# Kernel tuning notes

Hardware: AMD Instinct MI355X
Metric: run time of the kernel (lower is better)

## Reference

```python
import jax, jax.numpy as jnp
import numpy as np


def setup_inputs() -> dict:
    key = jax.random.key(0)
    k1, k2, k3 = jax.random.split(key, 3)
    D, L = 1024, 8192
    Bsz = 4
    h = jax.random.normal(k1, (D, L), dtype=jnp.float32)
    x = jax.random.normal(k2, (Bsz, D, L), dtype=jnp.float32)
    B = jax.random.normal(k3, (D, 1), dtype=jnp.float32)
    return {"h": h, "x": x, "B": B}


def reference(h, x, B):
    L = h.shape[-1]
    n = 2 * L  # zero-pad to 2L for linear (non-circular) convolution
    # torch rfft(norm='forward') divides by n; irfft(norm='forward') multiplies
    # by n — the factors cancel, and jnp supports the same norm argument.
    h_f = jnp.fft.rfft(h.astype(jnp.float32), n=n, norm="forward")  # [D, L+1]
    x_f = jnp.fft.rfft(x.astype(h.dtype), n=n)                      # [Bsz, D, L+1]
    y = jnp.fft.irfft(h_f * x_f, n=n, norm="forward")[..., :L]
    y = y + x * B  # B broadcasts [D,1] over [Bsz, D, L]
    return y.astype(x.dtype)
```

## Files before the change

kernel.cpp:

```cpp
#include <hip/hip_runtime.h>
#include <math.h>


#define FFT_N  8192
#define LOG_N  13
#define SEQ_L  8192
#define DIM_D  1024
#define NTHR   512

__device__ __forceinline__ float2 cadd(float2 a, float2 b){ return make_float2(a.x+b.x, a.y+b.y); }
__device__ __forceinline__ float2 csub(float2 a, float2 b){ return make_float2(a.x-b.x, a.y-b.y); }
__device__ __forceinline__ float2 cmul(float2 a, float2 b){ return make_float2(a.x*b.x - a.y*b.y, a.x*b.y + a.y*b.x); }
__device__ __forceinline__ int rev13(int k){ return (int)(__brev((unsigned)k) >> 19); }
__device__ __forceinline__ int SW(int i){ return i ^ ((i >> 5) & 15) ^ ((i >> 9) & 15); }

__device__ __forceinline__ void dif_pass4(float2 v[16], float2 w){
    {   constexpr float c8c[8] = {1.f, 0.92387953251f, 0.70710678119f, 0.38268343236f, 0.f, -0.38268343236f, -0.70710678119f, -0.92387953251f};
        constexpr float c8s[8] = {0.f, -0.38268343236f, -0.70710678119f, -0.92387953251f, -1.f, -0.92387953251f, -0.70710678119f, -0.38268343236f};
        #pragma unroll
        for (int m = 0; m < 8; ++m){
            float2 tw = cmul(make_float2(c8c[m], c8s[m]), w);
            float2 u = v[m], t = v[m+8];
            v[m] = cadd(u,t);
            v[m+8] = cmul(csub(u,t), tw);
        }
    }
    w = cmul(w,w);
    {   constexpr float c4c[4] = {1.f, 0.70710678119f, 0.f, -0.70710678119f};
        constexpr float c4s[4] = {0.f, -0.70710678119f, -1.f, -0.70710678119f};
        #pragma unroll
        for (int h = 0; h < 16; h += 8)
            #pragma unroll
            for (int m = 0; m < 4; ++m){
                float2 tw = cmul(make_float2(c4c[m], c4s[m]), w);
                float2 u = v[h+m], t = v[h+m+4];
                v[h+m] = cadd(u,t);
                v[h+m+4] = cmul(csub(u,t), tw);
            }
    }
    w = cmul(w,w);
    #pragma unroll
    for (int q = 0; q < 16; q += 4)
        #pragma unroll
        for (int m = 0; m < 2; ++m){
            float2 tw = (m == 0) ? w : make_float2(w.y, -w.x);
            float2 u = v[q+m], t = v[q+m+2];
            v[q+m] = cadd(u,t);
            v[q+m+2] = cmul(csub(u,t), tw);
        }
    w = cmul(w,w);
    #pragma unroll
    for (int e = 0; e < 16; e += 2){
        float2 u = v[e], t = v[e+1];
        v[e] = cadd(u,t);
        v[e+1] = cmul(csub(u,t), w);
    }
}

__device__ __forceinline__ void dit_pass4(float2 v[16], float2 w3){
    float2 w2 = cmul(w3,w3), w1 = cmul(w2,w2), w0 = cmul(w1,w1);
    #pragma unroll
    for (int e = 0; e < 16; e += 2){
        float2 t = cmul(v[e+1], w0);
        float2 u = v[e];
        v[e] = cadd(u,t); v[e+1] = csub(u,t);
    }
    #pragma unroll
    for (int q = 0; q < 16; q += 4)
        #pragma unroll
        for (int m = 0; m < 2; ++m){
            float2 tw = (m == 0) ? w1 : make_float2(-w1.y, w1.x);
            float2 t = cmul(v[q+m+2], tw);
            float2 u = v[q+m];
            v[q+m] = cadd(u,t); v[q+m+2] = csub(u,t);
        }
    {   constexpr float c4c[4] = {1.f, 0.70710678119f, 0.f, -0.70710678119f};
        constexpr float c4s[4] = {0.f, 0.70710678119f, 1.f, 0.70710678119f};
        #pragma unroll
        for (int h = 0; h < 16; h += 8)
            #pragma unroll
            for (int m = 0; m < 4; ++m){
                float2 tw = cmul(make_float2(c4c[m], c4s[m]), w2);
                float2 t = cmul(v[h+m+4], tw);
                float2 u = v[h+m];
                v[h+m] = cadd(u,t); v[h+m+4] = csub(u,t);
            }
    }
    {   constexpr float c8c[8] = {1.f, 0.92387953251f, 0.70710678119f, 0.38268343236f, 0.f, -0.38268343236f, -0.70710678119f, -0.92387953251f};
        constexpr float c8s[8] = {0.f, 0.38268343236f, 0.70710678119f, 0.92387953251f, 1.f, 0.92387953251f, 0.70710678119f, 0.38268343236f};
        #pragma unroll
        for (int m = 0; m < 8; ++m){
            float2 tw = cmul(make_float2(c8c[m], c8s[m]), w3);
            float2 t = cmul(v[m+8], tw);
            float2 u = v[m];
            v[m] = cadd(u,t); v[m+8] = csub(u,t);
        }
    }
}

__device__ __forceinline__ void fwd_fft12(float2* z, int tid){
    float2 v[16];
    float sn, cs;
    __sincosf(-(float)M_PI * (float)tid * (1.0f/4096.0f), &sn, &cs);
    float2 base = make_float2(cs, sn);
    #pragma unroll
    for (int k = 0; k < 16; ++k) v[k] = z[SW((k<<9) | tid)];
    dif_pass4(v, base);
    #pragma unroll
    for (int k = 0; k < 16; ++k) z[SW((k<<9) | tid)] = v[k];
    __syncthreads();
    const int hi = tid >> 5, lo = tid & 31;
    __sincosf(-(float)M_PI * (float)lo * (1.0f/256.0f), &sn, &cs);
    base = make_float2(cs, sn);
    #pragma unroll
    for (int k = 0; k < 16; ++k) v[k] = z[SW((hi<<9) | (k<<5) | lo)];
    dif_pass4(v, base);
    #pragma unroll
    for (int k = 0; k < 16; ++k) z[SW((hi<<9) | (k<<5) | lo)] = v[k];
    __syncthreads();
    const int h2 = tid >> 1, b0 = tid & 1;
    base = b0 ? make_float2(0.98078528040f, -0.19509032202f)
              : make_float2(1.f, 0.f);
    #pragma unroll
    for (int k = 0; k < 16; ++k) v[k] = z[SW((h2<<5) | (k<<1) | b0)];
    dif_pass4(v, base);
    #pragma unroll
    for (int k = 0; k < 16; ++k) z[SW((h2<<5) | (k<<1) | b0)] = v[k];
    __syncthreads();
}

__device__ __forceinline__ void untangle(float2 zk, float2 znk, float2 t, float2& A, float2& G){
    float2 E  = make_float2(0.5f*(zk.x+znk.x), 0.5f*(zk.y-znk.y));
    float2 O  = make_float2(0.5f*(zk.y+znk.y), -0.5f*(zk.x-znk.x));
    float2 tO = cmul(t, O);
    A = cadd(E, tO); G = csub(E, tO);
}

__device__ __forceinline__ void pointmul(float2 zk, float2 znk, float2 t,
                                         float2 Ah, float2 Gh, float invN,
                                         float2& Wp, float2& Wm){
    float2 Xp, Xm; untangle(zk, znk, t, Xp, Xm);
    float2 Cp = cmul(Ah, Xp), Cm = cmul(Gh, Xm);
    float2 S  = make_float2(0.5f*(Cp.x+Cm.x), 0.5f*(Cp.y+Cm.y));
    float2 Dd = make_float2(0.5f*(Cp.x-Cm.x), 0.5f*(Cp.y-Cm.y));
    float2 u  = make_float2(t.y*Dd.x - t.x*Dd.y, t.y*Dd.y + t.x*Dd.x);
    Wp = make_float2((S.x+u.x)*invN, (S.y+u.y)*invN);
    Wm = make_float2((S.x-u.x)*invN, -((S.y-u.y)*invN));
}

__global__ __launch_bounds__(NTHR)
void h_spec_kernel(const float* __restrict__ h,
                   float4* __restrict__ p0, float4* __restrict__ p1,
                   float2* __restrict__ hs2)
{
    __shared__ float2 z[FFT_N];
    const int tid = (int)threadIdx.x;
    const int d   = (int)blockIdx.x;
    const float2* hrow = (const float2*)(h + (size_t)d * SEQ_L);

    #pragma unroll
    for (int j = 0; j < 8; ++j){
        int n = tid + NTHR * j;
        z[SW(n)] = hrow[n];
        z[SW(n + FFT_N/2)] = make_float2(0.f, 0.f);
    }
    __syncthreads();
    fwd_fft12(z, tid);

    const size_t base = (size_t)d * 2048;
    #pragma unroll
    for (int q = 0; q < 4; ++q){
        int g = tid + NTHR * q;
        float2 A1, G1, A2, G2;
        if (g == 0){
            float2 z0 = z[SW(0)], z1 = z[SW(1)], z2 = z[SW(2)], z3 = z[SW(3)];
            float2 Z0 = cadd(z0,z1), Z1 = csub(z0,z1), Z2 = cadd(z2,z3), Z3 = csub(z2,z3);
            float2 A3, G3;
            untangle(Z0, Z0, make_float2(1.f, 0.f), A1, G1);
            untangle(Z2, Z3, make_float2(0.70710678119f, -0.70710678119f), A2, G2);
            untangle(Z1, Z1, make_float2(0.f, -1.f), A3, G3);
            hs2[(size_t)d*2 + 0] = A3;
            hs2[(size_t)d*2 + 1] = G3;
        } else {
            int a = rev13(g), c = rev13(4096 - g);
            float2 za = z[SW(a)], zb = z[SW(a+1)], zc = z[SW(c)], zd = z[SW(c+1)];
            float2 Z12a = cadd(za,zb), Z12b = csub(za,zb);
            float2 Z12c = cadd(zc,zd), Z12d = csub(zc,zd);
            float sn, cs; __sincosf(-(float)M_PI * (float)g * (1.0f/8192.0f), &sn, &cs);
            float2 t1 = make_float2(cs, sn), t2 = make_float2(-sn, -cs);
            untangle(Z12a, Z12d, t1, A1, G1);
            untangle(Z12c, Z12b, t2, A2, G2);
        }
        p0[base + q*NTHR + tid] = make_float4(A1.x, A1.y, G1.x, G1.y);
        p1[base + q*NTHR + tid] = make_float4(A2.x, A2.y, G2.x, G2.y);
    }
}

__global__ __launch_bounds__(NTHR)
void fftconv_x_kernel(const float* __restrict__ x,
                      const float* __restrict__ Bv,
                      float* __restrict__ y,
                      const float4* __restrict__ p0, const float4* __restrict__ p1,
                      const float2* __restrict__ hs2)
{
    __shared__ float2 z[FFT_N];
    const int tid = (int)threadIdx.x;
    const int d   = (int)blockIdx.x;
    const int b   = (int)blockIdx.y;

    const float Bd = Bv[d];
    const float2* xrow = (const float2*)(x + ((size_t)b * DIM_D + (size_t)d) * SEQ_L);
    float2*       yrow = (float2*)(y + ((size_t)b * DIM_D + (size_t)d) * SEQ_L);
    const float invN = 1.0f / (float)FFT_N;

    #pragma unroll
    for (int j = 0; j < 8; ++j){
        int n = tid + NTHR * j;
        z[SW(n)] = xrow[n];
        z[SW(n + FFT_N/2)] = make_float2(0.f, 0.f);
    }
    __syncthreads();
    fwd_fft12(z, tid);

    const size_t base = (size_t)d * 2048;
    #pragma unroll
    for (int q = 0; q < 4; ++q){
        int g = tid + NTHR * q;
        float4 f0 = p0[base + q*NTHR + tid];
        float4 f1 = p1[base + q*NTHR + tid];
        float2 Ah1 = make_float2(f0.x, f0.y), Gh1 = make_float2(f0.z, f0.w);
        float2 Ah2 = make_float2(f1.x, f1.y), Gh2 = make_float2(f1.z, f1.w);
        if (g == 0){
            float2 A3 = hs2[(size_t)d*2 + 0], G3 = hs2[(size_t)d*2 + 1];
            float2 z0 = z[SW(0)], z1 = z[SW(1)], z2 = z[SW(2)], z3 = z[SW(3)];
            float2 Z0 = cadd(z0,z1), Z1 = csub(z0,z1), Z2 = cadd(z2,z3), Z3 = csub(z2,z3);
            float2 W0, W0b, W1, W1b, W2, W3;
            pointmul(Z0, Z0, make_float2(1.f, 0.f),  Ah1, Gh1, invN, W0, W0b);
            pointmul(Z1, Z1, make_float2(0.f, -1.f), A3,  G3,  invN, W1, W1b);
            pointmul(Z2, Z3, make_float2(0.70710678119f, -0.70710678119f), Ah2, Gh2, invN, W2, W3);
            z[SW(0)] = cadd(W0, W1);
            z[SW(1)] = csub(W0, W1);
            z[SW(2)] = cadd(W2, W3);
            z[SW(3)] = csub(W2, W3);
        } else {
            int a = rev13(g), c = rev13(4096 - g);
            float2 za = z[SW(a)], zb = z[SW(a+1)], zc = z[SW(c)], zd = z[SW(c+1)];
            float2 Z12a = cadd(za,zb), Z12b = csub(za,zb);
            float2 Z12c = cadd(zc,zd), Z12d = csub(zc,zd);
            float sn, cs; __sincosf(-(float)M_PI * (float)g * (1.0f/8192.0f), &sn, &cs);
            float2 t1 = make_float2(cs, sn), t2 = make_float2(-sn, -cs);
            float2 Wp1, Wm1, Wp2, Wm2;
            pointmul(Z12a, Z12d, t1, Ah1, Gh1, invN, Wp1, Wm1);
            pointmul(Z12c, Z12b, t2, Ah2, Gh2, invN, Wp2, Wm2);
            z[SW(a)]   = cadd(Wp1, Wm2);
            z[SW(a+1)] = csub(Wp1, Wm2);
            z[SW(c)]   = cadd(Wp2, Wm1);
            z[SW(c+1)] = csub(Wp2, Wm1);
        }
    }
    __syncthreads();

    {
        float2 v[16];
        float sn, cs;
        const int h2 = tid >> 1, b0 = tid & 1, hi = tid >> 5, lo = tid & 31;
        float2 w3 = b0 ? make_float2(0.98078528040f, 0.19509032202f)
                       : make_float2(1.f, 0.f);
        #pragma unroll
        for (int k = 0; k < 16; ++k) v[k] = z[SW((h2<<5) | (k<<1) | b0)];
        dit_pass4(v, w3);
        #pragma unroll
        for (int k = 0; k < 16; ++k) z[SW((h2<<5) | (k<<1) | b0)] = v[k];
        __syncthreads();
        __sincosf((float)M_PI * (float)lo * (1.0f/256.0f), &sn, &cs);
        w3 = make_float2(cs, sn);
        #pragma unroll
        for (int k = 0; k < 16; ++k) v[k] = z[SW((hi<<9) | (k<<5) | lo)];
        dit_pass4(v, w3);
        #pragma unroll
        for (int k = 0; k < 16; ++k) z[SW((hi<<9) | (k<<5) | lo)] = v[k];
        __syncthreads();
        __sincosf((float)M_PI * (float)tid * (1.0f/4096.0f), &sn, &cs);
        w3 = make_float2(cs, sn);
        #pragma unroll
        for (int k = 0; k < 16; ++k) v[k] = z[SW((k<<9) | tid)];
        dit_pass4(v, w3);
        #pragma unroll
        for (int k = 0; k < 16; ++k) z[SW((k<<9) | tid)] = v[k];
        __syncthreads();
    }

    #pragma unroll
    for (int j = 0; j < 8; ++j){
        int n = tid + NTHR * j;
        float2 wv = z[SW(n)];
        float2 xv = xrow[n];
        yrow[n] = make_float2(wv.x + xv.x * Bd, wv.y + xv.y * Bd);
    }
}

__global__ __launch_bounds__(NTHR)
void fftconv_fused(const float* __restrict__ h,
                   const float* __restrict__ x,
                   const float* __restrict__ Bv,
                   float* __restrict__ y)
{
    __shared__ float2 z[FFT_N];
    const int tid = (int)threadIdx.x;
    const int d   = (int)blockIdx.x;
    const int b   = (int)blockIdx.y;

    const float Bd = Bv[d];
    const float2* hrow = (const float2*)(h + (size_t)d * SEQ_L);
    const float2* xrow = (const float2*)(x + ((size_t)b * DIM_D + (size_t)d) * SEQ_L);
    float2*       yrow = (float2*)(y + ((size_t)b * DIM_D + (size_t)d) * SEQ_L);
    const float invN = 1.0f / (float)FFT_N;

    #pragma unroll
    for (int j = 0; j < 8; ++j){
        int n = tid + NTHR * j;
        z[SW(n)] = hrow[n];
        z[SW(n + FFT_N/2)] = make_float2(0.f, 0.f);
    }
    __syncthreads();
    fwd_fft12(z, tid);

    float2 Ah1[4], Gh1[4], Ah2[4], Gh2[4], Ah3, Gh3;
    #pragma unroll
    for (int q = 0; q < 4; ++q){
        int g = tid + NTHR * q;
        if (g == 0){
            float2 z0 = z[SW(0)], z1 = z[SW(1)], z2 = z[SW(2)], z3 = z[SW(3)];
            float2 Z0 = cadd(z0,z1), Z1 = csub(z0,z1), Z2 = cadd(z2,z3), Z3 = csub(z2,z3);
            untangle(Z0, Z0, make_float2(1.f, 0.f), Ah1[0], Gh1[0]);
            untangle(Z2, Z3, make_float2(0.70710678119f, -0.70710678119f), Ah2[0], Gh2[0]);
            untangle(Z1, Z1, make_float2(0.f, -1.f), Ah3, Gh3);
        } else {
            int a = rev13(g), c = rev13(4096 - g);
            float2 za = z[SW(a)], zb = z[SW(a+1)], zc = z[SW(c)], zd = z[SW(c+1)];
            float2 Z12a = cadd(za,zb), Z12b = csub(za,zb);
            float2 Z12c = cadd(zc,zd), Z12d = csub(zc,zd);
            float sn, cs; __sincosf(-(float)M_PI * (float)g * (1.0f/8192.0f), &sn, &cs);
            float2 t1 = make_float2(cs, sn), t2 = make_float2(-sn, -cs);
            untangle(Z12a, Z12d, t1, Ah1[q], Gh1[q]);
            untangle(Z12c, Z12b, t2, Ah2[q], Gh2[q]);
        }
    }
    __syncthreads();

    #pragma unroll
    for (int j = 0; j < 8; ++j){
        int n = tid + NTHR * j;
        z[SW(n)] = xrow[n];
        z[SW(n + FFT_N/2)] = make_float2(0.f, 0.f);
    }
    __syncthreads();
    fwd_fft12(z, tid);

    #pragma unroll
    for (int q = 0; q < 4; ++q){
        int g = tid + NTHR * q;
        if (g == 0){
            float2 z0 = z[SW(0)], z1 = z[SW(1)], z2 = z[SW(2)], z3 = z[SW(3)];
            float2 Z0 = cadd(z0,z1), Z1 = csub(z0,z1), Z2 = cadd(z2,z3), Z3 = csub(z2,z3);
            float2 W0, W0b, W1, W1b, W2, W3;
            pointmul(Z0, Z0, make_float2(1.f, 0.f),  Ah1[0], Gh1[0], invN, W0, W0b);
            pointmul(Z1, Z1, make_float2(0.f, -1.f), Ah3,    Gh3,    invN, W1, W1b);
            pointmul(Z2, Z3, make_float2(0.70710678119f, -0.70710678119f), Ah2[0], Gh2[0], invN, W2, W3);
            z[SW(0)] = cadd(W0, W1);
            z[SW(1)] = csub(W0, W1);
            z[SW(2)] = cadd(W2, W3);
            z[SW(3)] = csub(W2, W3);
        } else {
            int a = rev13(g), c = rev13(4096 - g);
            float2 za = z[SW(a)], zb = z[SW(a+1)], zc = z[SW(c)], zd = z[SW(c+1)];
            float2 Z12a = cadd(za,zb), Z12b = csub(za,zb);
            float2 Z12c = cadd(zc,zd), Z12d = csub(zc,zd);
            float sn, cs; __sincosf(-(float)M_PI * (float)g * (1.0f/8192.0f), &sn, &cs);
            float2 t1 = make_float2(cs, sn), t2 = make_float2(-sn, -cs);
            float2 Wp1, Wm1, Wp2, Wm2;
            pointmul(Z12a, Z12d, t1, Ah1[q], Gh1[q], invN, Wp1, Wm1);
            pointmul(Z12c, Z12b, t2, Ah2[q], Gh2[q], invN, Wp2, Wm2);
            z[SW(a)]   = cadd(Wp1, Wm2);
            z[SW(a+1)] = csub(Wp1, Wm2);
            z[SW(c)]   = cadd(Wp2, Wm1);
            z[SW(c+1)] = csub(Wp2, Wm1);
        }
    }
    __syncthreads();

    {
        float2 v[16];
        float sn, cs;
        const int h2 = tid >> 1, b0 = tid & 1, hi = tid >> 5, lo = tid & 31;
        float2 w3 = b0 ? make_float2(0.98078528040f, 0.19509032202f)
                       : make_float2(1.f, 0.f);
        #pragma unroll
        for (int k = 0; k < 16; ++k) v[k] = z[SW((h2<<5) | (k<<1) | b0)];
        dit_pass4(v, w3);
        #pragma unroll
        for (int k = 0; k < 16; ++k) z[SW((h2<<5) | (k<<1) | b0)] = v[k];
        __syncthreads();
        __sincosf((float)M_PI * (float)lo * (1.0f/256.0f), &sn, &cs);
        w3 = make_float2(cs, sn);
        #pragma unroll
        for (int k = 0; k < 16; ++k) v[k] = z[SW((hi<<9) | (k<<5) | lo)];
        dit_pass4(v, w3);
        #pragma unroll
        for (int k = 0; k < 16; ++k) z[SW((hi<<9) | (k<<5) | lo)] = v[k];
        __syncthreads();
        __sincosf((float)M_PI * (float)tid * (1.0f/4096.0f), &sn, &cs);
        w3 = make_float2(cs, sn);
        #pragma unroll
        for (int k = 0; k < 16; ++k) v[k] = z[SW((k<<9) | tid)];
        dit_pass4(v, w3);
        #pragma unroll
        for (int k = 0; k < 16; ++k) z[SW((k<<9) | tid)] = v[k];
        __syncthreads();
    }

    #pragma unroll
    for (int j = 0; j < 8; ++j){
        int n = tid + NTHR * j;
        float2 wv = z[SW(n)];
        float2 xv = xrow[n];
        yrow[n] = make_float2(wv.x + xv.x * Bd, wv.y + xv.y * Bd);
    }
}

extern "C" void kernel_launch(void* const* d_in, const int* in_sizes, int n_in,
                              void* d_out, int out_size, void* d_ws, size_t ws_size,
                              hipStream_t stream) {
    const float* h  = (const float*)d_in[0];
    const float* x  = (const float*)d_in[1];
    const float* Bv = (const float*)d_in[2];
    float* y = (float*)d_out;

    const int bsz = out_size / (DIM_D * SEQ_L);
    const size_t plane = (size_t)DIM_D * 2048;
    const size_t need  = plane * 2 * sizeof(float4) + (size_t)DIM_D * 2 * sizeof(float2);

    if (ws_size >= need) {
        float4* p0  = (float4*)d_ws;
        float4* p1  = p0 + plane;
        float2* hs2 = (float2*)(p1 + plane);
        hipLaunchKernelGGL(h_spec_kernel, dim3(DIM_D), dim3(NTHR), 0, stream, h, p0, p1, hs2);
        hipLaunchKernelGGL(fftconv_x_kernel, dim3(DIM_D, bsz), dim3(NTHR), 0, stream,
                           x, Bv, y, p0, p1, hs2);
    } else {
        hipLaunchKernelGGL(fftconv_fused, dim3(DIM_D, bsz), dim3(NTHR), 0, stream, h, x, Bv, y);
    }
}
```

Before: 408.3 us.

## Fuse global load into first FFT pass and epilogue into last pass

The first radix-16 DIF pass now reads the input row directly from global memory into registers. Because the upper half of the input is zero padding, that first stage reduces to a twiddle multiply, so no zero-filled shared-memory load or extra barrier is needed. The final inverse pass writes y = conv + x*B straight from registers, and in the batched kernel it reuses the input values kept in registers instead of re-reading x. Swizzle index math is specialised per pass and trivial twiddles are special-cased. This removes one shared-memory round trip and two barriers per FFT, at the cost of higher register pressure from the saved x values.

Result: faster. 378.1 us (-7.4%).

```diff
diff --git a/kernel.cpp b/kernel.cpp
--- a/kernel.cpp
+++ b/kernel.cpp
@@ -3,7 +3,6 @@
 
 
 #define FFT_N  8192
-#define LOG_N  13
 #define SEQ_L  8192
 #define DIM_D  1024
 #define NTHR   512
@@ -14,47 +13,63 @@
 __device__ __forceinline__ int rev13(int k){ return (int)(__brev((unsigned)k) >> 19); }
 __device__ __forceinline__ int SW(int i){ return i ^ ((i >> 5) & 15) ^ ((i >> 9) & 15); }
 
+__device__ __forceinline__ float2 tw8_dif(int m, float2 w){
+    constexpr float c[8] = {1.f, 0.92387953251f, 0.70710678119f, 0.38268343236f, 0.f, -0.38268343236f, -0.70710678119f, -0.92387953251f};
+    constexpr float s[8] = {0.f, -0.38268343236f, -0.70710678119f, -0.92387953251f, -1.f, -0.92387953251f, -0.70710678119f, -0.38268343236f};
+    if (m == 0) return w;
+    if (m == 4) return make_float2(w.y, -w.x);
+    return cmul(make_float2(c[m], s[m]), w);
+}
+__device__ __forceinline__ float2 tw8_dit(int m, float2 w){
+    constexpr float c[8] = {1.f, 0.92387953251f, 0.70710678119f, 0.38268343236f, 0.f, -0.38268343236f, -0.70710678119f, -0.92387953251f};
+    constexpr float s[8] = {0.f, 0.38268343236f, 0.70710678119f, 0.92387953251f, 1.f, 0.92387953251f, 0.70710678119f, 0.38268343236f};
+    if (m == 0) return w;
+    if (m == 4) return make_float2(-w.y, w.x);
+    return cmul(make_float2(c[m], s[m]), w);
+}
+
+__device__ __forceinline__ void dif_stage8(float2 v[16], float2 w){
+    #pragma unroll
+    for (int m = 0; m < 8; ++m){
+        float2 tw = tw8_dif(m, w);
+        float2 u = v[m], t = v[m+8];
+        v[m] = cadd(u,t);
+        v[m+8] = cmul(csub(u,t), tw);
+    }
+}
+
+__device__ __forceinline__ void dif_tail3(float2 v[16], float2 w){
+    {
+        float2 t0 = w;
+        float2 t1 = cmul(make_float2(0.70710678119f, -0.70710678119f), w);
+        float2 t2 = make_float2(w.y, -w.x);
+        float2 t3 = cmul(make_float2(-0.70710678119f, -0.70710678119f), w);
+        #pragma unroll
+        for (int h = 0; h < 16; h += 8){
+            { float2 u=v[h+0], t=v[h+4]; v[h+0]=cadd(u,t); v[h+4]=cmul(csub(u,t), t0); }
+            { float2 u=v[h+1], t=v[h+5]; v[h+1]=cadd(u,t); v[h+5]=cmul(csub(u,t), t1); }
+            { float2 u=v[h+2], t=v[h+6]; v[h+2]=cadd(u,t); v[h+6]=cmul(csub(u,t), t2); }
+            { float2 u=v[h+3], t=v[h+7]; v[h+3]=cadd(u,t); v[h+7]=cmul(csub(u,t), t3); }
+        }
+    }
+    w = cmul(w,w);
+    #pragma unroll
+    for (int q = 0; q < 16; q += 4){
+        { float2 u=v[q+0], t=v[q+2]; v[q+0]=cadd(u,t); v[q+2]=cmul(csub(u,t), w); }
+        { float2 u=v[q+1], t=v[q+3]; float2 tw=make_float2(w.y,-w.x);
+          v[q+1]=cadd(u,t); v[q+3]=cmul(csub(u,t), tw); }
+    }
+    w = cmul(w,w);
+    #pragma unroll
+    for (int e = 0; e < 16; e += 2){
+        float2 u=v[e], t=v[e+1];
+        v[e]=cadd(u,t); v[e+1]=cmul(csub(u,t), w);
+    }
+}
+
 __device__ __forceinline__ void dif_pass4(float2 v[16], float2 w){
-    {   constexpr float c8c[8] = {1.f, 0.92387953251f, 0.70710678119f, 0.38268343236f, 0.f, -0.38268343236f, -0.70710678119f, -0.92387953251f};
-        constexpr float c8s[8] = {0.f, -0.38268343236f, -0.70710678119f, -0.92387953251f, -1.f, -0.92387953251f, -0.70710678119f, -0.38268343236f};
-        #pragma unroll
-        for (int m = 0; m < 8; ++m){
-            float2 tw = cmul(make_float2(c8c[m], c8s[m]), w);
-            float2 u = v[m], t = v[m+8];
-            v[m] = cadd(u,t);
-            v[m+8] = cmul(csub(u,t), tw);
-        }
-    }
-    w = cmul(w,w);
-    {   constexpr float c4c[4] = {1.f, 0.70710678119f, 0.f, -0.70710678119f};
-        constexpr float c4s[4] = {0.f, -0.70710678119f, -1.f, -0.70710678119f};
-        #pragma unroll
-        for (int h = 0; h < 16; h += 8)
-            #pragma unroll
-            for (int m = 0; m < 4; ++m){
-                float2 tw = cmul(make_float2(c4c[m], c4s[m]), w);
-                float2 u = v[h+m], t = v[h+m+4];
-                v[h+m] = cadd(u,t);
-                v[h+m+4] = cmul(csub(u,t), tw);
-            }
-    }
-    w = cmul(w,w);
-    #pragma unroll
-    for (int q = 0; q < 16; q += 4)
-        #pragma unroll
-        for (int m = 0; m < 2; ++m){
-            float2 tw = (m == 0) ? w : make_float2(w.y, -w.x);
-            float2 u = v[q+m], t = v[q+m+2];
-            v[q+m] = cadd(u,t);
-            v[q+m+2] = cmul(csub(u,t), tw);
-        }
-    w = cmul(w,w);
-    #pragma unroll
-    for (int e = 0; e < 16; e += 2){
-        float2 u = v[e], t = v[e+1];
-        v[e] = cadd(u,t);
-        v[e+1] = cmul(csub(u,t), w);
-    }
+    dif_stage8(v, w);
+    dif_tail3(v, cmul(w,w));
 }
 
 __device__ __forceinline__ void dit_pass4(float2 v[16], float2 w3){
@@ -66,66 +81,72 @@
         v[e] = cadd(u,t); v[e+1] = csub(u,t);
     }
     #pragma unroll
-    for (int q = 0; q < 16; q += 4)
-        #pragma unroll
-        for (int m = 0; m < 2; ++m){
-            float2 tw = (m == 0) ? w1 : make_float2(-w1.y, w1.x);
-            float2 t = cmul(v[q+m+2], tw);
-            float2 u = v[q+m];
-            v[q+m] = cadd(u,t); v[q+m+2] = csub(u,t);
-        }
-    {   constexpr float c4c[4] = {1.f, 0.70710678119f, 0.f, -0.70710678119f};
-        constexpr float c4s[4] = {0.f, 0.70710678119f, 1.f, 0.70710678119f};
-        #pragma unroll
-        for (int h = 0; h < 16; h += 8)
-            #pragma unroll
-            for (int m = 0; m < 4; ++m){
-                float2 tw = cmul(make_float2(c4c[m], c4s[m]), w2);
-                float2 t = cmul(v[h+m+4], tw);
-                float2 u = v[h+m];
-                v[h+m] = cadd(u,t); v[h+m+4] = csub(u,t);
-            }
-    }
-    {   constexpr float c8c[8] = {1.f, 0.92387953251f, 0.70710678119f, 0.38268343236f, 0.f, -0.38268343236f, -0.70710678119f, -0.92387953251f};
-        constexpr float c8s[8] = {0.f, 0.38268343236f, 0.70710678119f, 0.92387953251f, 1.f, 0.92387953251f, 0.70710678119f, 0.38268343236f};
-        #pragma unroll
-        for (int m = 0; m < 8; ++m){
-            float2 tw = cmul(make_float2(c8c[m], c8s[m]), w3);
-            float2 t = cmul(v[m+8], tw);
-            float2 u = v[m];
-            v[m] = cadd(u,t); v[m+8] = csub(u,t);
-        }
-    }
-}
-
-__device__ __forceinline__ void fwd_fft12(float2* z, int tid){
+    for (int q = 0; q < 16; q += 4){
+        { float2 t = cmul(v[q+2], w1); float2 u=v[q+0]; v[q+0]=cadd(u,t); v[q+2]=csub(u,t); }
+        { float2 tw = make_float2(-w1.y, w1.x);
+          float2 t = cmul(v[q+3], tw); float2 u=v[q+1]; v[q+1]=cadd(u,t); v[q+3]=csub(u,t); }
+    }
+    {   float2 t0 = w2;
+        float2 t1 = cmul(make_float2(0.70710678119f, 0.70710678119f), w2);
+        float2 t2 = make_float2(-w2.y, w2.x);
+        float2 t3 = cmul(make_float2(-0.70710678119f, 0.70710678119f), w2);
+        #pragma unroll
+        for (int h = 0; h < 16; h += 8){
+            { float2 t=cmul(v[h+4], t0); float2 u=v[h+0]; v[h+0]=cadd(u,t); v[h+4]=csub(u,t); }
+            { float2 t=cmul(v[h+5], t1); float2 u=v[h+1]; v[h+1]=cadd(u,t); v[h+5]=csub(u,t); }
+            { float2 t=cmul(v[h+6], t2); float2 u=v[h+2]; v[h+2]=cadd(u,t); v[h+6]=csub(u,t); }
+            { float2 t=cmul(v[h+7], t3); float2 u=v[h+3]; v[h+3]=cadd(u,t); v[h+7]=csub(u,t); }
+        }
+    }
+    #pragma unroll
+    for (int m = 0; m < 8; ++m){
+        float2 tw = tw8_dit(m, w3);
+        float2 t = cmul(v[m+8], tw);
+        float2 u = v[m];
+        v[m] = cadd(u,t); v[m+8] = csub(u,t);
+    }
+}
+
+template<bool SAVEX>
+__device__ __forceinline__ void fwd_fft12_fused(float2* z, const float2* __restrict__ row,
+                                                int tid, float2* xs){
     float2 v[16];
     float sn, cs;
     __sincosf(-(float)M_PI * (float)tid * (1.0f/4096.0f), &sn, &cs);
-    float2 base = make_float2(cs, sn);
-    #pragma unroll
-    for (int k = 0; k < 16; ++k) v[k] = z[SW((k<<9) | tid)];
-    dif_pass4(v, base);
-    #pragma unroll
-    for (int k = 0; k < 16; ++k) z[SW((k<<9) | tid)] = v[k];
-    __syncthreads();
+    float2 w = make_float2(cs, sn);
+    const int T1 = tid ^ ((tid >> 5) & 15);
+    #pragma unroll
+    for (int k = 0; k < 8; ++k){
+        v[k] = row[(k<<9) | tid];
+        if (SAVEX) xs[k] = v[k];
+    }
+    #pragma unroll
+    for (int m = 0; m < 8; ++m) v[m+8] = cmul(v[m], tw8_dif(m, w));
+    dif_tail3(v, cmul(w,w));
+    #pragma unroll
+    for (int k = 0; k < 16; ++k) z[(k<<9) | (T1 ^ k)] = v[k];
+    __syncthreads();
+
     const int hi = tid >> 5, lo = tid & 31;
+    const int baseB = hi << 9, TB = lo ^ hi;
     __sincosf(-(float)M_PI * (float)lo * (1.0f/256.0f), &sn, &cs);
-    base = make_float2(cs, sn);
-    #pragma unroll
-    for (int k = 0; k < 16; ++k) v[k] = z[SW((hi<<9) | (k<<5) | lo)];
-    dif_pass4(v, base);
-    #pragma unroll
-    for (int k = 0; k < 16; ++k) z[SW((hi<<9) | (k<<5) | lo)] = v[k];
-    __syncthreads();
+    w = make_float2(cs, sn);
+    #pragma unroll
+    for (int k = 0; k < 16; ++k) v[k] = z[baseB | (k<<5) | (TB ^ k)];
+    dif_pass4(v, w);
+    #pragma unroll
+    for (int k = 0; k < 16; ++k) z[baseB | (k<<5) | (TB ^ k)] = v[k];
+    __syncthreads();
+
     const int h2 = tid >> 1, b0 = tid & 1;
-    base = b0 ? make_float2(0.98078528040f, -0.19509032202f)
-              : make_float2(1.f, 0.f);
-    #pragma unroll
-    for (int k = 0; k < 16; ++k) v[k] = z[SW((h2<<5) | (k<<1) | b0)];
-    dif_pass4(v, base);
-    #pragma unroll
-    for (int k = 0; k < 16; ++k) z[SW((h2<<5) | (k<<1) | b0)] = v[k];
+    const int baseC = h2 << 5, M3 = (h2 ^ (h2 >> 4)) & 15;
+    w = b0 ? make_float2(0.98078528040f, -0.19509032202f)
+           : make_float2(1.f, 0.f);
+    #pragma unroll
+    for (int k = 0; k < 16; ++k) v[k] = z[baseC | (((k<<1)|b0) ^ M3)];
+    dif_pass4(v, w);
+    #pragma unroll
+    for (int k = 0; k < 16; ++k) z[baseC | (((k<<1)|b0) ^ M3)] = v[k];
     __syncthreads();
 }
 
@@ -158,14 +179,8 @@
     const int d   = (int)blockIdx.x;
     const float2* hrow = (const float2*)(h + (size_t)d * SEQ_L);
 
-    #pragma unroll
-    for (int j = 0; j < 8; ++j){
-        int n = tid + NTHR * j;
-        z[SW(n)] = hrow[n];
-        z[SW(n + FFT_N/2)] = make_float2(0.f, 0.f);
-    }
-    __syncthreads();
-    fwd_fft12(z, tid);
+    float2 dummy[8];
+    fwd_fft12_fused<false>(z, hrow, tid, dummy);
 
     const size_t base = (size_t)d * 2048;
     #pragma unroll
@@ -213,14 +228,8 @@
     float2*       yrow = (float2*)(y + ((size_t)b * DIM_D + (size_t)d) * SEQ_L);
     const float invN = 1.0f / (float)FFT_N;
 
-    #pragma unroll
-    for (int j = 0; j < 8; ++j){
-        int n = tid + NTHR * j;
-        z[SW(n)] = xrow[n];
-        z[SW(n + FFT_N/2)] = make_float2(0.f, 0.f);
-    }
-    __syncthreads();
-    fwd_fft12(z, tid);
+    float2 xs[8];
+    fwd_fft12_fused<true>(z, xrow, tid, xs);
 
     const size_t base = (size_t)d * 2048;
     #pragma unroll
@@ -264,38 +273,35 @@
         float2 v[16];
         float sn, cs;
         const int h2 = tid >> 1, b0 = tid & 1, hi = tid >> 5, lo = tid & 31;
+        const int baseC = h2 << 5, M3 = (h2 ^ (h2 >> 4)) & 15;
         float2 w3 = b0 ? make_float2(0.98078528040f, 0.19509032202f)
                        : make_float2(1.f, 0.f);
         #pragma unroll
-        for (int k = 0; k < 16; ++k) v[k] = z[SW((h2<<5) | (k<<1) | b0)];
-        dit_pass4(v, w3);
-        #pragma unroll
-        for (int k = 0; k < 16; ++k) z[SW((h2<<5) | (k<<1) | b0)] = v[k];
+        for (int k = 0; k < 16; ++k) v[k] = z[baseC | (((k<<1)|b0) ^ M3)];
+        dit_pass4(v, w3);
+        #pragma unroll
+        for (int k = 0; k < 16; ++k) z[baseC | (((k<<1)|b0) ^ M3)] = v[k];
         __syncthreads();
+        const int baseB = hi << 9, TB = lo ^ hi;
         __sincosf((float)M_PI * (float)lo * (1.0f/256.0f), &sn, &cs);
         w3 = make_float2(cs, sn);
         #pragma unroll
-        for (int k = 0; k < 16; ++k) v[k] = z[SW((hi<<9) | (k<<5) | lo)];
-        dit_pass4(v, w3);
-        #pragma unroll
-        for (int k = 0; k < 16; ++k) z[SW((hi<<9) | (k<<5) | lo)] = v[k];
+        for (int k = 0; k < 16; ++k) v[k] = z[baseB | (k<<5) | (TB ^ k)];
+        dit_pass4(v, w3);
+        #pragma unroll
+        for (int k = 0; k < 16; ++k) z[baseB | (k<<5) | (TB ^ k)] = v[k];
         __syncthreads();
+        const int T1 = tid ^ ((tid >> 5) & 15);
         __sincosf((float)M_PI * (float)tid * (1.0f/4096.0f), &sn, &cs);
         w3 = make_float2(cs, sn);
         #pragma unroll
-        for (int k = 0; k < 16; ++k) v[k] = z[SW((k<<9) | tid)];
-        dit_pass4(v, w3);
-        #pragma unroll
-        for (int k = 0; k < 16; ++k) z[SW((k<<9) | tid)] = v[k];
-        __syncthreads();
-    }
-
-    #pragma unroll
-    for (int j = 0; j < 8; ++j){
-        int n = tid + NTHR * j;
-        float2 wv = z[SW(n)];
-        float2 xv = xrow[n];
-        yrow[n] = make_float2(wv.x + xv.x * Bd, wv.y + xv.y * Bd);
+        for (int k = 0; k < 16; ++k) v[k] = z[(k<<9) | (T1 ^ k)];
+        dit_pass4(v, w3);
+        #pragma unroll
+        for (int k = 0; k < 8; ++k){
+            int n = (k<<9) | tid;
+            yrow[n] = make_float2(v[k].x + xs[k].x * Bd, v[k].y + xs[k].y * Bd);
+        }
     }
 }
 
@@ -316,14 +322,8 @@
     float2*       yrow = (float2*)(y + ((size_t)b * DIM_D + (size_t)d) * SEQ_L);
     const float invN = 1.0f / (float)FFT_N;
 
-    #pragma unroll
-    for (int j = 0; j < 8; ++j){
-        int n = tid + NTHR * j;
-        z[SW(n)] = hrow[n];
-        z[SW(n + FFT_N/2)] = make_float2(0.f, 0.f);
-    }
-    __syncthreads();
-    fwd_fft12(z, tid);
+    float2 dummy[8];
+    fwd_fft12_fused<false>(z, hrow, tid, dummy);
 
     float2 Ah1[4], Gh1[4], Ah2[4], Gh2[4], Ah3, Gh3;
     #pragma unroll
@@ -348,14 +348,7 @@
     }
     __syncthreads();
 
-    #pragma unroll
-    for (int j = 0; j < 8; ++j){
-        int n = tid + NTHR * j;
-        z[SW(n)] = xrow[n];
-        z[SW(n + FFT_N/2)] = make_float2(0.f, 0.f);
-    }
-    __syncthreads();
-    fwd_fft12(z, tid);
+    fwd_fft12_fused<false>(z, xrow, tid, dummy);
 
     #pragma unroll
     for (int q = 0; q < 4; ++q){
@@ -393,38 +386,36 @@
         float2 v[16];
         float sn, cs;
         const int h2 = tid >> 1, b0 = tid & 1, hi = tid >> 5, lo = tid & 31;
+        const int baseC = h2 << 5, M3 = (h2 ^ (h2 >> 4)) & 15;
         float2 w3 = b0 ? make_float2(0.98078528040f, 0.19509032202f)
                        : make_float2(1.f, 0.f);
         #pragma unroll
-        for (int k = 0; k < 16; ++k) v[k] = z[SW((h2<<5) | (k<<1) | b0)];
-        dit_pass4(v, w3);
-        #pragma unroll
-        for (int k = 0; k < 16; ++k) z[SW((h2<<5) | (k<<1) | b0)] = v[k];
+        for (int k = 0; k < 16; ++k) v[k] = z[baseC | (((k<<1)|b0) ^ M3)];
+        dit_pass4(v, w3);
+        #pragma unroll
+        for (int k = 0; k < 16; ++k) z[baseC | (((k<<1)|b0) ^ M3)] = v[k];
         __syncthreads();
+        const int baseB = hi << 9, TB = lo ^ hi;
         __sincosf((float)M_PI * (float)lo * (1.0f/256.0f), &sn, &cs);
         w3 = make_float2(cs, sn);
         #pragma unroll
-        for (int k = 0; k < 16; ++k) v[k] = z[SW((hi<<9) | (k<<5) | lo)];
-        dit_pass4(v, w3);
-        #pragma unroll
-        for (int k = 0; k < 16; ++k) z[SW((hi<<9) | (k<<5) | lo)] = v[k];
+        for (int k = 0; k < 16; ++k) v[k] = z[baseB | (k<<5) | (TB ^ k)];
+        dit_pass4(v, w3);
+        #pragma unroll
+        for (int k = 0; k < 16; ++k) z[baseB | (k<<5) | (TB ^ k)] = v[k];
         __syncthreads();
+        const int T1 = tid ^ ((tid >> 5) & 15);
         __sincosf((float)M_PI * (float)tid * (1.0f/4096.0f), &sn, &cs);
         w3 = make_float2(cs, sn);
         #pragma unroll
-        for (int k = 0; k < 16; ++k) v[k] = z[SW((k<<9) | tid)];
-        dit_pass4(v, w3);
-        #pragma unroll
-        for (int k = 0; k < 16; ++k) z[SW((k<<9) | tid)] = v[k];
-        __syncthreads();
-    }
-
-    #pragma unroll
-    for (int j = 0; j < 8; ++j){
-        int n = tid + NTHR * j;
-        float2 wv = z[SW(n)];
-        float2 xv = xrow[n];
-        yrow[n] = make_float2(wv.x + xv.x * Bd, wv.y + xv.y * Bd);
+        for (int k = 0; k < 16; ++k) v[k] = z[(k<<9) | (T1 ^ k)];
+        dit_pass4(v, w3);
+        #pragma unroll
+        for (int k = 0; k < 8; ++k){
+            int n = (k<<9) | tid;
+            float2 xv = xrow[n];
+            yrow[n] = make_float2(v[k].x + xv.x * Bd, v[k].y + xv.y * Bd);
+        }
     }
 }
 
```
